# Kernel tuning notes

Hardware: AMD Instinct MI355X
Metric: run time of the kernel (lower is better)

## Reference

```python
import jax, jax.numpy as jnp
import numpy as np

B, S, D_IN = 2, 2048, 1024
HIDDEN, H, HKV = 1024, 16, 4
R = H // HKV          # query heads per kv head
HD = HIDDEN // H      # head_dim = 64
D_OUT = 1024
SCALE = HD ** -0.5


def setup_inputs() -> dict:
    key = jax.random.key(0)
    ks = jax.random.split(key, 5)
    x = jax.random.normal(ks[0], (B, S, D_IN), dtype=jnp.float32)
    # store weights as (in, out); torch Linear computes x @ W.T with W (out,in)
    Wq = jax.random.normal(ks[1], (D_IN, HIDDEN), dtype=jnp.float32) * 0.02
    Wk = jax.random.normal(ks[2], (D_IN, HKV * HD), dtype=jnp.float32) * 0.02
    Wv = jax.random.normal(ks[3], (D_IN, HKV * HD), dtype=jnp.float32) * 0.02
    Wo = jax.random.normal(ks[4], (HIDDEN, D_OUT), dtype=jnp.float32) * 0.02
    return {"x": x, "Wq": Wq, "Wk": Wk, "Wv": Wv, "Wo": Wo}


def reference(x, Wq, Wk, Wv, Wo):
    # projections
    q = x @ Wq                                   # (B,S,H*HD)
    k = x @ Wk                                   # (B,S,HKV*HD)
    v = x @ Wv
    # repeat_interleave maps query head h -> kv head h // R,
    # so split query heads as (HKV, R) groups and broadcast KV.
    q = q.reshape(B, S, HKV, R, HD)
    k = k.reshape(B, S, HKV, HD)
    v = v.reshape(B, S, HKV, HD)
    attn = jnp.einsum('bskrd,btkd->bkrst', q, k) * SCALE   # (B,HKV,R,S,S)
    attn = jax.nn.softmax(attn, axis=-1)
    o = jnp.einsum('bkrst,btkd->bskrd', attn, v)           # (B,S,HKV,R,HD)
    o = o.reshape(B, S, HIDDEN)
    return o @ Wo                                          # (B,S,D_OUT)
```

## Files before the change

### kernel.cpp

```cpp
#include <hip/hip_runtime.h>

using u16 = unsigned short;
using u32 = unsigned int;
typedef __bf16 bf16x8 __attribute__((ext_vector_type(8)));
typedef u16 u16x8 __attribute__((ext_vector_type(8)));
typedef u32 u32x2 __attribute__((ext_vector_type(2)));
typedef u32 u32x4 __attribute__((ext_vector_type(4)));
typedef float f32x4 __attribute__((ext_vector_type(4)));
typedef float f32x16 __attribute__((ext_vector_type(16)));

#define B_   2
#define S_   2048
#define DIN  1024
#define HID  1024
#define NH   16
#define NKV  4
#define HD_  64
#define QKVW 1536
#define QSCL 0.1803368801111244f

__device__ __forceinline__ u16 f2b(float f) {
  u32 u = __builtin_bit_cast(u32, f);
  u32 r = (u + 0x7FFFu + ((u >> 16) & 1u)) >> 16;
  return (u16)r;
}

__device__ __forceinline__ void gl16(const void* g, void* l) {
  __builtin_amdgcn_global_load_lds(
      (const __attribute__((address_space(1))) void*)g,
      (__attribute__((address_space(3))) void*)l, 16, 0, 0);
}

__global__ void k_cvt(const float* __restrict__ in, u16* __restrict__ out, int n8) {
  int i = blockIdx.x * 256 + threadIdx.x;
  if (i >= n8) return;
  const float4* p = (const float4*)(in + (size_t)i * 8);
  float4 a = p[0], b = p[1];
  u16x8 o;
  o[0] = f2b(a.x); o[1] = f2b(a.y); o[2] = f2b(a.z); o[3] = f2b(a.w);
  o[4] = f2b(b.x); o[5] = f2b(b.y); o[6] = f2b(b.z); o[7] = f2b(b.w);
  *(u16x8*)(out + (size_t)i * 8) = o;
}

__global__ __launch_bounds__(256) void k_cvt_t(const float* __restrict__ W, u16* __restrict__ WT, int K, int N) {
  __shared__ float t[32][33];
  const int k0 = blockIdx.x * 32, n0 = blockIdx.y * 32;
  const int c = threadIdx.x & 31, r8 = threadIdx.x >> 5;
#pragma unroll
  for (int i = 0; i < 4; ++i)
    t[r8 + i * 8][c] = W[(size_t)(k0 + r8 + i * 8) * N + n0 + c];
  __syncthreads();
#pragma unroll
  for (int i = 0; i < 4; ++i)
    WT[(size_t)(n0 + r8 + i * 8) * K + k0 + c] = f2b(t[c][r8 + i * 8]);
}

template <typename OutT>
__global__ __launch_bounds__(256, 2) void k_gemm_bt(
    const u16* __restrict__ A, const u16* __restrict__ Bt,
    OutT* __restrict__ C, int M, int N, int K, int scaleCols, float scl)
{
  __shared__ u16 lA[2][128 * 32];
  __shared__ u16 lB[2][128 * 32];
  const int tid  = threadIdx.x;
  const int lane = tid & 63;
  const int wave = tid >> 6;
  const int wm = wave >> 1, wn = wave & 1;
  const int g = lane >> 4, li = lane & 15;
  const int bm = blockIdx.y * 128, bn = blockIdx.x * 128;
  const int srow = wave * 16 + (lane >> 2);
  const int scol = (lane & 3) * 8;

  f32x4 acc[4][4];
#pragma unroll
  for (int i = 0; i < 4; ++i)
#pragma unroll
    for (int j = 0; j < 4; ++j) acc[i][j] = f32x4{0.f, 0.f, 0.f, 0.f};

  const u16* Ab = A + (size_t)bm * K;
  const u16* Bb = Bt + (size_t)bn * K;

#pragma unroll
  for (int h = 0; h < 2; ++h) {
    gl16(&Ab[(size_t)(h * 64 + srow) * K + scol], (char*)lA[0] + h * 4096 + wave * 1024);
    gl16(&Bb[(size_t)(h * 64 + srow) * K + scol], (char*)lB[0] + h * 4096 + wave * 1024);
  }
  __syncthreads();

  int cur = 0;
  for (int k0 = 0; k0 < K; k0 += 32) {
    if (k0 + 32 < K) {
#pragma unroll
      for (int h = 0; h < 2; ++h) {
        gl16(&Ab[(size_t)(h * 64 + srow) * K + k0 + 32 + scol], (char*)lA[cur ^ 1] + h * 4096 + wave * 1024);
        gl16(&Bb[(size_t)(h * 64 + srow) * K + k0 + 32 + scol], (char*)lB[cur ^ 1] + h * 4096 + wave * 1024);
      }
    }
    bf16x8 af[4], bfr[4];
#pragma unroll
    for (int mt = 0; mt < 4; ++mt)
      af[mt] = *(const bf16x8*)&lA[cur][(wm * 64 + mt * 16 + li) * 32 + g * 8];
#pragma unroll
    for (int nt = 0; nt < 4; ++nt)
      bfr[nt] = *(const bf16x8*)&lB[cur][(wn * 64 + nt * 16 + li) * 32 + g * 8];
    __builtin_amdgcn_s_setprio(1);
#pragma unroll
    for (int mt = 0; mt < 4; ++mt)
#pragma unroll
      for (int nt = 0; nt < 4; ++nt)
        acc[mt][nt] = __builtin_amdgcn_mfma_f32_16x16x32_bf16(af[mt], bfr[nt], acc[mt][nt], 0, 0, 0);
    __builtin_amdgcn_s_setprio(0);
    __syncthreads();
    cur ^= 1;
  }

#pragma unroll
  for (int mt = 0; mt < 4; ++mt)
#pragma unroll
    for (int nt = 0; nt < 4; ++nt)
#pragma unroll
      for (int r = 0; r < 4; ++r) {
        int row = bm + wm * 64 + mt * 16 + g * 4 + r;
        int col = bn + wn * 64 + nt * 16 + li;
        float v = acc[mt][nt][r];
        if (col < scaleCols) v *= scl;
        if constexpr (sizeof(OutT) == 4) C[(size_t)row * N + col] = v;
        else                             C[(size_t)row * N + col] = f2b(v);
      }
}

__global__ __launch_bounds__(256, 2) void k_attn(
    const u16* __restrict__ QKV, u16* __restrict__ O)
{
  __shared__ u16 K_lds[2][64 * 64];
  __shared__ u16 Vt_lds[2][64 * 64];
  const int tid  = threadIdx.x;
  const int lane = tid & 63;
  const int w    = tid >> 6;
  const int lq = lane & 31;
  const int hi = lane >> 5;
  const int swl = (lq & 7) << 3;
  const int hx = (hi * 8) ^ (swl & 8);
  const int s0 = blockIdx.x * 32;
  const int kv = blockIdx.y;
  const int b  = blockIdx.z;
  const int hq = kv * 4 + w;

  int dcol[4];
#pragma unroll
  for (int d0 = 0; d0 < 4; ++d0) dcol[d0] = (d0 * 16) ^ (swl & 48);

  bf16x8 qf[4];
  {
    const u16* qb = QKV + (size_t)(b * S_ + s0 + lq) * QKVW + hq * HD_ + hi * 8;
#pragma unroll
    for (int d0 = 0; d0 < 4; ++d0) qf[d0] = *(const bf16x8*)(qb + d0 * 16);
  }

  float l = 0.f;
  f32x16 oacc0 = {}, oacc1 = {};

  const int kt = tid >> 3, kc = (tid & 7) * 8;
  const u16* kgb = QKV + (size_t)(b * S_ + kt) * QKVW + HID + kv * HD_ + kc;
  const int vt = tid & 63, vd = (tid >> 6) * 8;
  const u16* vgb = QKV + (size_t)(b * S_ + vt) * QKVW + HID + NKV * HD_ + kv * HD_ + vd;
  const int kdst = kt * 64 + (kc ^ ((kt & 7) << 3));

  {
    u16x8 ka = *(const u16x8*)(kgb);
    u16x8 kb = *(const u16x8*)(kgb + (size_t)32 * QKVW);
    u16x8 va = *(const u16x8*)(vgb);
    u16x8 vb = *(const u16x8*)(vgb + 32);
    *(u16x8*)&K_lds[0][kdst]           = ka;
    *(u16x8*)&K_lds[0][kdst + 32 * 64] = kb;
#pragma unroll
    for (int e = 0; e < 8; ++e) {
      const int sz = (vt ^ (((vd + e) & 7) << 3));
      Vt_lds[0][(vd + e) * 64 + sz]      = va[e];
      Vt_lds[0][(vd + 32 + e) * 64 + sz] = vb[e];
    }
  }
  __syncthreads();

  constexpr int NT = S_ / 64;
  for (int t = 0; t < NT; ++t) {
    const int cur = t & 1;
    u16x8 ka, kb, va, vb;
    const bool pref = (t + 1 < NT);
    if (pref) {
      const u16* kp = kgb + (size_t)(t + 1) * 64 * QKVW;
      const u16* vp = vgb + (size_t)(t + 1) * 64 * QKVW;
      ka = *(const u16x8*)(kp);
      kb = *(const u16x8*)(kp + (size_t)32 * QKVW);
      va = *(const u16x8*)(vp);
      vb = *(const u16x8*)(vp + 32);
    }

    f32x16 st0 = {}, st1 = {};
    __builtin_amdgcn_s_setprio(1);
#pragma unroll
    for (int d0 = 0; d0 < 4; ++d0) {
      bf16x8 kf0 = *(const bf16x8*)&K_lds[cur][lq * 64 + dcol[d0] + hx];
      bf16x8 kf1 = *(const bf16x8*)&K_lds[cur][(32 + lq) * 64 + dcol[d0] + hx];
      st0 = __builtin_amdgcn_mfma_f32_32x32x16_bf16(kf0, qf[d0], st0, 0, 0, 0);
      st1 = __builtin_amdgcn_mfma_f32_32x32x16_bf16(kf1, qf[d0], st1, 0, 0, 0);
    }
    __builtin_amdgcn_s_setprio(0);

#pragma unroll
    for (int i = 0; i < 16; ++i) st0[i] = __builtin_amdgcn_exp2f(st0[i]);
#pragma unroll
    for (int i = 0; i < 16; ++i) st1[i] = __builtin_amdgcn_exp2f(st1[i]);
    float s8[8];
#pragma unroll
    for (int i = 0; i < 8; ++i)
      s8[i] = (st0[i] + st0[i + 8]) + (st1[i] + st1[i + 8]);
    s8[0] += s8[4]; s8[1] += s8[5]; s8[2] += s8[6]; s8[3] += s8[7];
    l += (s8[0] + s8[1]) + (s8[2] + s8[3]);

    bf16x8 pa[4];
#define PK(dst, x, y) asm("v_cvt_pk_bf16_f32 %0, %1, %2" : "=v"(dst) : "v"(x), "v"(y))
#pragma unroll
    for (int kb2 = 0; kb2 < 2; ++kb2) {
      const f32x16& ev = kb2 ? st1 : st0;
      u32 a0, a1, b0, b1;
      u32x2 r0, r1;
      u32x4 wv;
      PK(a0, ev[0], ev[1]);  PK(a1, ev[2], ev[3]);
      PK(b0, ev[4], ev[5]);  PK(b1, ev[6], ev[7]);
      r0 = __builtin_amdgcn_permlane32_swap(a0, b0, false, false);
      r1 = __builtin_amdgcn_permlane32_swap(a1, b1, false, false);
      wv[0] = r0[0]; wv[1] = r1[0]; wv[2] = r0[1]; wv[3] = r1[1];
      pa[kb2 * 2] = __builtin_bit_cast(bf16x8, wv);
      PK(a0, ev[8],  ev[9]);  PK(a1, ev[10], ev[11]);
      PK(b0, ev[12], ev[13]); PK(b1, ev[14], ev[15]);
      r0 = __builtin_amdgcn_permlane32_swap(a0, b0, false, false);
      r1 = __builtin_amdgcn_permlane32_swap(a1, b1, false, false);
      wv[0] = r0[0]; wv[1] = r1[0]; wv[2] = r0[1]; wv[3] = r1[1];
      pa[kb2 * 2 + 1] = __builtin_bit_cast(bf16x8, wv);
    }
#undef PK

    __builtin_amdgcn_s_setprio(1);
#pragma unroll
    for (int ks = 0; ks < 4; ++ks) {
      bf16x8 vf0 = *(const bf16x8*)&Vt_lds[cur][lq * 64 + dcol[ks] + hx];
      bf16x8 vf1 = *(const bf16x8*)&Vt_lds[cur][(32 + lq) * 64 + dcol[ks] + hx];
      oacc0 = __builtin_amdgcn_mfma_f32_32x32x16_bf16(pa[ks], vf0, oacc0, 0, 0, 0);
      oacc1 = __builtin_amdgcn_mfma_f32_32x32x16_bf16(pa[ks], vf1, oacc1, 0, 0, 0);
    }
    __builtin_amdgcn_s_setprio(0);

    if (pref) {
      *(u16x8*)&K_lds[cur ^ 1][kdst]           = ka;
      *(u16x8*)&K_lds[cur ^ 1][kdst + 32 * 64] = kb;
#pragma unroll
      for (int e = 0; e < 8; ++e) {
        const int sz = (vt ^ (((vd + e) & 7) << 3));
        Vt_lds[cur ^ 1][(vd + e) * 64 + sz]      = va[e];
        Vt_lds[cur ^ 1][(vd + 32 + e) * 64 + sz] = vb[e];
      }
    }
    __syncthreads();
  }

  l += __shfl_xor(l, 32);
  const size_t obase = (size_t)(b * S_ + s0) * HID + hq * HD_ + lq;
#pragma unroll
  for (int r = 0; r < 16; ++r) {
    const int qrow = (r & 3) + 8 * (r >> 2) + 4 * hi;
    float lr = __shfl(l, qrow);
    float inv = __builtin_amdgcn_rcpf(lr);
    O[obase + (size_t)qrow * HID]      = f2b(oacc0[r] * inv);
    O[obase + (size_t)qrow * HID + 32] = f2b(oacc1[r] * inv);
  }
}

extern "C" void kernel_launch(void* const* d_in, const int* in_sizes, int n_in,
                              void* d_out, int out_size, void* d_ws, size_t ws_size,
                              hipStream_t stream) {
  (void)in_sizes; (void)n_in; (void)out_size; (void)ws_size;
  const float* x  = (const float*)d_in[0];
  const float* Wq = (const float*)d_in[1];
  const float* Wk = (const float*)d_in[2];
  const float* Wv = (const float*)d_in[3];
  const float* Wo = (const float*)d_in[4];
  float* out = (float*)d_out;

  const size_t M = (size_t)B_ * S_;
  u16* xb    = (u16*)d_ws;
  u16* WqkvT = xb    + M * DIN;
  u16* WoT   = WqkvT + (size_t)QKVW * DIN;
  u16* QKV   = WoT   + (size_t)HID * HID;
  u16* Ob    = QKV   + M * QKVW;

  k_cvt<<<dim3((int)(M * DIN / 8 / 256)), 256, 0, stream>>>(x, xb, (int)(M * DIN / 8));
  k_cvt_t<<<dim3(DIN / 32, HID / 32),       256, 0, stream>>>(Wq, WqkvT,                      DIN, HID);
  k_cvt_t<<<dim3(DIN / 32, (NKV*HD_) / 32), 256, 0, stream>>>(Wk, WqkvT + (size_t)HID * DIN,  DIN, NKV * HD_);
  k_cvt_t<<<dim3(DIN / 32, (NKV*HD_) / 32), 256, 0, stream>>>(Wv, WqkvT + (size_t)(HID + NKV*HD_) * DIN, DIN, NKV * HD_);
  k_cvt_t<<<dim3(HID / 32, HID / 32),       256, 0, stream>>>(Wo, WoT, HID, HID);

  k_gemm_bt<u16><<<dim3(QKVW / 128, (int)(M / 128)), 256, 0, stream>>>(
      xb, WqkvT, QKV, (int)M, QKVW, DIN, HID, QSCL);

  k_attn<<<dim3(S_ / 32, NKV, B_), 256, 0, stream>>>(QKV, Ob);

  k_gemm_bt<float><<<dim3(HID / 128, (int)(M / 128)), 256, 0, stream>>>(
      Ob, WoT, out, (int)M, HID, HID, 0, 1.0f);
}
```

Before: 115.5 us.

## Pre-transpose V globally and stage K/V tiles via direct-to-LDS loads; shrink GEMM N-tile

Adds a kernel that writes V transposed per (batch, kv head) into workspace. The attention kernel can then stage both K and V^T tiles with direct global-to-LDS loads instead of register round-trips and scalar transposing LDS writes. The GEMM tile is narrowed to 128x64 with a higher occupancy hint, roughly doubling the grid to fill more CUs. This costs an extra kernel launch and an extra pass over V, and the new staging uses a different XOR swizzle that must match the existing fragment reads.

Measured after the change: 110.7 us. -4.2%, faster.

```diff
diff --git a/kernel.cpp b/kernel.cpp
--- a/kernel.cpp
+++ b/kernel.cpp
@@ -55,59 +55,72 @@
     WT[(size_t)(n0 + r8 + i * 8) * K + k0 + c] = f2b(t[c][r8 + i * 8]);
 }
 
+__global__ __launch_bounds__(256) void k_vt(const u16* __restrict__ QKV, u16* __restrict__ Vt) {
+  __shared__ u16 t[32][33];
+  const int s0 = blockIdx.x * 32;
+  const int d0 = blockIdx.y * 32;
+  const int z  = blockIdx.z;
+  const int b = z >> 2, kv = z & 3;
+  const int c = threadIdx.x & 31, r8 = threadIdx.x >> 5;
+#pragma unroll
+  for (int i = 0; i < 4; ++i)
+    t[r8 + i * 8][c] = QKV[(size_t)(b * S_ + s0 + r8 + i * 8) * QKVW + (HID + NKV * HD_) + kv * HD_ + d0 + c];
+  __syncthreads();
+#pragma unroll
+  for (int i = 0; i < 4; ++i)
+    Vt[(size_t)(z * HD_ + d0 + r8 + i * 8) * S_ + s0 + c] = t[c][r8 + i * 8];
+}
+
 template <typename OutT>
-__global__ __launch_bounds__(256, 2) void k_gemm_bt(
+__global__ __launch_bounds__(256, 4) void k_gemm_bt(
     const u16* __restrict__ A, const u16* __restrict__ Bt,
     OutT* __restrict__ C, int M, int N, int K, int scaleCols, float scl)
 {
   __shared__ u16 lA[2][128 * 32];
-  __shared__ u16 lB[2][128 * 32];
+  __shared__ u16 lB[2][64 * 32];
   const int tid  = threadIdx.x;
   const int lane = tid & 63;
   const int wave = tid >> 6;
   const int wm = wave >> 1, wn = wave & 1;
   const int g = lane >> 4, li = lane & 15;
-  const int bm = blockIdx.y * 128, bn = blockIdx.x * 128;
-  const int srow = wave * 16 + (lane >> 2);
-  const int scol = (lane & 3) * 8;
-
-  f32x4 acc[4][4];
-#pragma unroll
-  for (int i = 0; i < 4; ++i)
-#pragma unroll
-    for (int j = 0; j < 4; ++j) acc[i][j] = f32x4{0.f, 0.f, 0.f, 0.f};
+  const int bm = blockIdx.y * 128, bn = blockIdx.x * 64;
+  const int arow = wave * 16 + (lane >> 2);
+  const int acol = (lane & 3) * 8;
+
+  f32x4 acc[4][2];
+#pragma unroll
+  for (int i = 0; i < 4; ++i)
+#pragma unroll
+    for (int j = 0; j < 2; ++j) acc[i][j] = f32x4{0.f, 0.f, 0.f, 0.f};
 
   const u16* Ab = A + (size_t)bm * K;
   const u16* Bb = Bt + (size_t)bn * K;
 
-#pragma unroll
-  for (int h = 0; h < 2; ++h) {
-    gl16(&Ab[(size_t)(h * 64 + srow) * K + scol], (char*)lA[0] + h * 4096 + wave * 1024);
-    gl16(&Bb[(size_t)(h * 64 + srow) * K + scol], (char*)lB[0] + h * 4096 + wave * 1024);
-  }
+  auto stage = [&](int k0, int buf) {
+#pragma unroll
+    for (int h = 0; h < 2; ++h)
+      gl16(&Ab[(size_t)(h * 64 + arow) * K + k0 + acol], (char*)lA[buf] + h * 4096 + wave * 1024);
+    gl16(&Bb[(size_t)arow * K + k0 + acol], (char*)lB[buf] + wave * 1024);
+  };
+
+  stage(0, 0);
   __syncthreads();
 
   int cur = 0;
   for (int k0 = 0; k0 < K; k0 += 32) {
-    if (k0 + 32 < K) {
-#pragma unroll
-      for (int h = 0; h < 2; ++h) {
-        gl16(&Ab[(size_t)(h * 64 + srow) * K + k0 + 32 + scol], (char*)lA[cur ^ 1] + h * 4096 + wave * 1024);
-        gl16(&Bb[(size_t)(h * 64 + srow) * K + k0 + 32 + scol], (char*)lB[cur ^ 1] + h * 4096 + wave * 1024);
-      }
-    }
-    bf16x8 af[4], bfr[4];
+    if (k0 + 32 < K) stage(k0 + 32, cur ^ 1);
+    bf16x8 af[4], bfr[2];
 #pragma unroll
     for (int mt = 0; mt < 4; ++mt)
       af[mt] = *(const bf16x8*)&lA[cur][(wm * 64 + mt * 16 + li) * 32 + g * 8];
 #pragma unroll
-    for (int nt = 0; nt < 4; ++nt)
-      bfr[nt] = *(const bf16x8*)&lB[cur][(wn * 64 + nt * 16 + li) * 32 + g * 8];
+    for (int nt = 0; nt < 2; ++nt)
+      bfr[nt] = *(const bf16x8*)&lB[cur][(wn * 32 + nt * 16 + li) * 32 + g * 8];
     __builtin_amdgcn_s_setprio(1);
 #pragma unroll
     for (int mt = 0; mt < 4; ++mt)
 #pragma unroll
-      for (int nt = 0; nt < 4; ++nt)
+      for (int nt = 0; nt < 2; ++nt)
         acc[mt][nt] = __builtin_amdgcn_mfma_f32_16x16x32_bf16(af[mt], bfr[nt], acc[mt][nt], 0, 0, 0);
     __builtin_amdgcn_s_setprio(0);
     __syncthreads();
@@ -117,11 +130,11 @@
 #pragma unroll
   for (int mt = 0; mt < 4; ++mt)
 #pragma unroll
-    for (int nt = 0; nt < 4; ++nt)
+    for (int nt = 0; nt < 2; ++nt)
 #pragma unroll
       for (int r = 0; r < 4; ++r) {
         int row = bm + wm * 64 + mt * 16 + g * 4 + r;
-        int col = bn + wn * 64 + nt * 16 + li;
+        int col = bn + wn * 32 + nt * 16 + li;
         float v = acc[mt][nt][r];
         if (col < scaleCols) v *= scl;
         if constexpr (sizeof(OutT) == 4) C[(size_t)row * N + col] = v;
@@ -130,7 +143,7 @@
 }
 
 __global__ __launch_bounds__(256, 2) void k_attn(
-    const u16* __restrict__ QKV, u16* __restrict__ O)
+    const u16* __restrict__ QKV, const u16* __restrict__ Vt_g, u16* __restrict__ O)
 {
   __shared__ u16 K_lds[2][64 * 64];
   __shared__ u16 Vt_lds[2][64 * 64];
@@ -160,41 +173,29 @@
   float l = 0.f;
   f32x16 oacc0 = {}, oacc1 = {};
 
-  const int kt = tid >> 3, kc = (tid & 7) * 8;
-  const u16* kgb = QKV + (size_t)(b * S_ + kt) * QKVW + HID + kv * HD_ + kc;
-  const int vt = tid & 63, vd = (tid >> 6) * 8;
-  const u16* vgb = QKV + (size_t)(b * S_ + vt) * QKVW + HID + NKV * HD_ + kv * HD_ + vd;
-  const int kdst = kt * 64 + (kc ^ ((kt & 7) << 3));
-
-  {
-    u16x8 ka = *(const u16x8*)(kgb);
-    u16x8 kb = *(const u16x8*)(kgb + (size_t)32 * QKVW);
-    u16x8 va = *(const u16x8*)(vgb);
-    u16x8 vb = *(const u16x8*)(vgb + 32);
-    *(u16x8*)&K_lds[0][kdst]           = ka;
-    *(u16x8*)&K_lds[0][kdst + 32 * 64] = kb;
-#pragma unroll
-    for (int e = 0; e < 8; ++e) {
-      const int sz = (vt ^ (((vd + e) & 7) << 3));
-      Vt_lds[0][(vd + e) * 64 + sz]      = va[e];
-      Vt_lds[0][(vd + 32 + e) * 64 + sz] = vb[e];
+  const int sr8 = lane >> 3;
+  const int scol = ((lane & 7) ^ sr8) * 8;
+  const int srow = w * 16;
+  const u16* kge = QKV + (size_t)(b * S_) * QKVW + HID + kv * HD_;
+  const u16* vge = Vt_g + (size_t)((b * NKV + kv) * HD_) * S_;
+
+  auto stage = [&](int t, int buf) {
+#pragma unroll
+    for (int h = 0; h < 2; ++h) {
+      gl16(kge + (size_t)(t * 64 + srow + h * 8 + sr8) * QKVW + scol,
+           (char*)K_lds[buf] + srow * 128 + h * 1024);
+      gl16(vge + (size_t)(srow + h * 8 + sr8) * S_ + t * 64 + scol,
+           (char*)Vt_lds[buf] + srow * 128 + h * 1024);
     }
-  }
+  };
+
+  stage(0, 0);
   __syncthreads();
 
   constexpr int NT = S_ / 64;
   for (int t = 0; t < NT; ++t) {
     const int cur = t & 1;
-    u16x8 ka, kb, va, vb;
-    const bool pref = (t + 1 < NT);
-    if (pref) {
-      const u16* kp = kgb + (size_t)(t + 1) * 64 * QKVW;
-      const u16* vp = vgb + (size_t)(t + 1) * 64 * QKVW;
-      ka = *(const u16x8*)(kp);
-      kb = *(const u16x8*)(kp + (size_t)32 * QKVW);
-      va = *(const u16x8*)(vp);
-      vb = *(const u16x8*)(vp + 32);
-    }
+    if (t + 1 < NT) stage(t + 1, cur ^ 1);
 
     f32x16 st0 = {}, st1 = {};
     __builtin_amdgcn_s_setprio(1);
@@ -251,16 +252,6 @@
     }
     __builtin_amdgcn_s_setprio(0);
 
-    if (pref) {
-      *(u16x8*)&K_lds[cur ^ 1][kdst]           = ka;
-      *(u16x8*)&K_lds[cur ^ 1][kdst + 32 * 64] = kb;
-#pragma unroll
-      for (int e = 0; e < 8; ++e) {
-        const int sz = (vt ^ (((vd + e) & 7) << 3));
-        Vt_lds[cur ^ 1][(vd + e) * 64 + sz]      = va[e];
-        Vt_lds[cur ^ 1][(vd + 32 + e) * 64 + sz] = vb[e];
-      }
-    }
     __syncthreads();
   }
 
@@ -293,6 +284,7 @@
   u16* WoT   = WqkvT + (size_t)QKVW * DIN;
   u16* QKV   = WoT   + (size_t)HID * HID;
   u16* Ob    = QKV   + M * QKVW;
+  u16* Vt    = Ob    + M * HID;
 
   k_cvt<<<dim3((int)(M * DIN / 8 / 256)), 256, 0, stream>>>(x, xb, (int)(M * DIN / 8));
   k_cvt_t<<<dim3(DIN / 32, HID / 32),       256, 0, stream>>>(Wq, WqkvT,                      DIN, HID);
@@ -300,11 +292,13 @@
   k_cvt_t<<<dim3(DIN / 32, (NKV*HD_) / 32), 256, 0, stream>>>(Wv, WqkvT + (size_t)(HID + NKV*HD_) * DIN, DIN, NKV * HD_);
   k_cvt_t<<<dim3(HID / 32, HID / 32),       256, 0, stream>>>(Wo, WoT, HID, HID);
 
-  k_gemm_bt<u16><<<dim3(QKVW / 128, (int)(M / 128)), 256, 0, stream>>>(
+  k_gemm_bt<u16><<<dim3(QKVW / 64, (int)(M / 128)), 256, 0, stream>>>(
       xb, WqkvT, QKV, (int)M, QKVW, DIN, HID, QSCL);
 
-  k_attn<<<dim3(S_ / 32, NKV, B_), 256, 0, stream>>>(QKV, Ob);
-
-  k_gemm_bt<float><<<dim3(HID / 128, (int)(M / 128)), 256, 0, stream>>>(
+  k_vt<<<dim3(S_ / 32, HD_ / 32, B_ * NKV), 256, 0, stream>>>(QKV, Vt);
+
+  k_attn<<<dim3(S_ / 32, NKV, B_), 256, 0, stream>>>(QKV, Vt, Ob);
+
+  k_gemm_bt<float><<<dim3(HID / 64, (int)(M / 128)), 256, 0, stream>>>(
       Ob, WoT, out, (int)M, HID, HID, 0, 1.0f);
 }
```
